# Performance work log

Measured on AMD Instinct MI355X. Metric: run time of the kernel, lower is better.

Reference implementation:

```python
import jax, jax.numpy as jnp
import numpy as np

N = 20000       # nodes
C = 64          # channels per irrep
E = 320000      # edges (avg degree 16)
S = 64          # num_species
R = 8           # radial embedding dim
HR = 64         # radial MLP hidden
HEADS = 2       # readout heads
AVG = 16.0      # avg_num_neighbors
SOFT = 2.0      # soft_normalization


def setup_inputs() -> dict:
    key = jax.random.key(0)
    ks = jax.random.split(key, 28)
    g = lambda k, sh, sc=1.0: jax.random.normal(k, sh, dtype=jnp.float32) * sc
    inv = lambda n: 1.0 / float(np.sqrt(n))
    return {
        "edge_vectors": g(ks[0], (E, 3)),
        "node_feats_s": g(ks[1], (N, C)),
        "node_feats_v": g(ks[2], (N, C, 3)),
        "radial_embeddings": g(ks[3], (E, R)),
        "node_species": jax.random.randint(ks[4], (N,), 0, S),
        "senders": jax.random.randint(ks[5], (E,), 0, N),
        "receivers": jax.random.randint(ks[6], (E,), 0, N),
        # residual FullyConnectedTensorProduct(feats, one-hot species) weights
        "W_rs": g(ks[7], (S, C, C), inv(C)),
        "W_rv": g(ks[8], (S, C, C), inv(C)),
        # interaction: linear up, radial MLP (5 TP paths), linear down
        "W_up_s": g(ks[9], (C, C), inv(C)),
        "W_up_v": g(ks[10], (C, C), inv(C)),
        "Wr1": g(ks[11], (R, HR), inv(R)),
        "Wr2": g(ks[12], (HR, 5 * C), inv(HR)),
        "W_down_s": g(ks[13], (C, C), inv(C)),
        "W_down_v": g(ks[14], (C, C), inv(C)),
        # equivariant product basis: per-channel species-indexed symmetric-contraction weights
        "w1s": g(ks[15], (S, C)),
        "w1v": g(ks[16], (S, C)),
        "w2ss": g(ks[17], (S, C)),
        "w2vv": g(ks[18], (S, C)),
        "w2sv": g(ks[19], (S, C)),
        "W_prod_s": g(ks[20], (C, C), inv(C)),
        "W_prod_v": g(ks[21], (C, C), inv(C)),
        # linear readout heads (out_irreps -> 1x0e per head)
        "w_read": g(ks[22], (HEADS, C), inv(C)),
    }


def reference(edge_vectors, node_feats_s, node_feats_v, radial_embeddings,
              node_species, senders, receivers,
              W_rs, W_rv, W_up_s, W_up_v, Wr1, Wr2, W_down_s, W_down_v,
              w1s, w1v, w2ss, w2vv, w2sv, W_prod_s, W_prod_v, w_read):
    n_nodes = node_feats_s.shape[0]
    sp = node_species

    # --- residual connection: FCTP(feats, one-hot(species)) == species-indexed channel mix
    res_s = jnp.einsum('nc,ncd->nd', node_feats_s, W_rs[sp])
    res_v = jnp.einsum('ncx,ncd->ndx', node_feats_v, W_rv[sp])

    # --- InteractionBlock ---
    s_u = node_feats_s @ W_up_s
    v_u = jnp.einsum('ncx,cd->ndx', node_feats_v, W_up_v)
    nrm = jnp.linalg.norm(edge_vectors, axis=-1, keepdims=True)
    u = edge_vectors / jnp.maximum(nrm, 1e-9)  # l=1 spherical harmonic direction [E,3]
    # radial MLP -> per-edge per-channel weights for the 5 CG paths of (0e+1o)x(0e+1o)->0e+1o
    w = (jax.nn.silu(radial_embeddings @ Wr1) @ Wr2).reshape(-1, 5, s_u.shape[1])
    se = s_u[senders]            # [E,C] gather (irregular)
    ve = v_u[senders]            # [E,C,3]
    dot = jnp.einsum('ecx,ex->ec', ve, u)          # 1o x 1o -> 0e
    crs = jnp.cross(ve, u[:, None, :])             # 1o x 1o -> 1o
    m_s = w[:, 0] * se + w[:, 3] * dot
    m_v = (w[:, 1][..., None] * ve
           + w[:, 2][..., None] * u[:, None, :]
           + w[:, 4][..., None] * crs)
    a_s = jax.ops.segment_sum(m_s, receivers, num_segments=n_nodes) / AVG
    a_v = jax.ops.segment_sum(m_v, receivers, num_segments=n_nodes) / AVG
    a_s = a_s @ W_down_s
    a_v = jnp.einsum('ncx,cd->ndx', a_v, W_down_v)

    # --- EquivariantProductBasisBlock: symmetric contraction (correlation<=2), per-channel
    # species-indexed weights, followed by a linear to out_irreps ---
    vv = jnp.sum(a_v * a_v, axis=-1)                                   # 1o (x) 1o -> 0e
    p_s = w1s[sp] * a_s + w2ss[sp] * a_s * a_s + w2vv[sp] * vv
    p_v = w1v[sp][..., None] * a_v + w2sv[sp][..., None] * a_s[..., None] * a_v
    p_s = p_s @ W_prod_s
    p_v = jnp.einsum('ncx,cd->ndx', p_v, W_prod_v)

    # --- soft normalization: phi(n) = 1/(1 + n*sus(n)), n = norm/SOFT ---
    def sus(x):
        return jnp.where(x > 0, jnp.exp(-1.0 / jnp.where(x > 0, x, 1.0)), 0.0)

    def phi(n):
        n = n / SOFT
        return 1.0 / (1.0 + n * sus(n))

    f_s = p_s * phi(jnp.abs(p_s))
    f_v = p_v * phi(jnp.linalg.norm(p_v, axis=-1, keepdims=True))

    # --- residual add ---
    f_s = f_s + res_s
    f_v = f_v + res_v

    # --- readout heads (Linear out_irreps -> 1x0e), stacked on axis=1 ---
    node_out = jnp.einsum('nc,hc->nh', f_s, w_read)
    return (node_out, f_s, f_v)
```

## Files before the change

### kernel.cpp

```cpp
#include <hip/hip_runtime.h>

#define N_NODES 20000
#define C 64
#define E_EDGES 320000
#define S_SPEC 64
#define R_DIM 8
#define HR 64
#define HEADS 2
#define TE 64
#define NPAIR (E_EDGES/128)
#define HPAD 68
#define INV_AVG (1.0f/16.0f)

#define FS_OFF 40000
#define FV_OFF 1320000

typedef short bf16x4 __attribute__((ext_vector_type(4)));
typedef float f32x4  __attribute__((ext_vector_type(4)));

__device__ __forceinline__ unsigned short f2bf(float f){
  unsigned u = __float_as_uint(f);
  u += 0x7fffu + ((u >> 16) & 1u);
  return (unsigned short)(u >> 16);
}
__device__ __forceinline__ float bf2f(unsigned short b){
  return __uint_as_float(((unsigned)b) << 16);
}
__device__ __forceinline__ unsigned packbf(float a, float b){
  return (unsigned)f2bf(a) | ((unsigned)f2bf(b) << 16);
}
__device__ __forceinline__ float unplo(unsigned u){ return __uint_as_float(u << 16); }
__device__ __forceinline__ float unphi(unsigned u){ return __uint_as_float(u & 0xffff0000u); }
__device__ __forceinline__ float phi_f(float x){
  float n = x * 0.5f;
  float s = (n > 0.0f) ? expf(-1.0f/n) : 0.0f;
  return 1.0f / (1.0f + n * s);
}

__global__ __launch_bounds__(256) void wr2t_kernel(const float* __restrict__ Wr2,
                                                   unsigned short* __restrict__ wr2t){
  int idx = blockIdx.x*256 + threadIdx.x;
  int n = idx >> 6, k = idx & 63;
  wr2t[idx] = f2bf(Wr2[k*320 + n] * INV_AVG);
}

__global__ __launch_bounds__(256) void wpack_kernel(
    const float* __restrict__ W_rs, const float* __restrict__ W_rv,
    const float* __restrict__ W_ds, const float* __restrict__ W_dv,
    const float* __restrict__ W_ps, const float* __restrict__ W_pv,
    const float* __restrict__ Wus,  const float* __restrict__ Wuv,
    unsigned* __restrict__ wrp, unsigned* __restrict__ wdp,
    unsigned* __restrict__ wpp, unsigned* __restrict__ wup){
  int idx = blockIdx.x*256 + threadIdx.x;
  if (idx < S_SPEC*C*C){
    wrp[idx] = packbf(W_rs[idx], W_rv[idx]);
  } else {
    int r = idx - S_SPEC*C*C;
    int which = r >> 12, e = r & 4095;
    if (which == 0)      wdp[e] = packbf(W_ds[e], W_dv[e]);
    else if (which == 1) wpp[e] = packbf(W_ps[e], W_pv[e]);
    else                 wup[e] = packbf(Wus[e],  Wuv[e]);
  }
}

__global__ __launch_bounds__(256) void node_up_kernel(
    const float* __restrict__ fs, const float* __restrict__ fv,
    const unsigned* __restrict__ wup,
    ushort4* __restrict__ suv){
  const int ni = threadIdx.x >> 6;
  const int d  = threadIdx.x & 63;
  const int n  = blockIdx.x*4 + ni;
  __shared__ float s_l[4][C];
  __shared__ float v_l[4][3][C];
  __shared__ unsigned wup_l[C*C];
  const int t = threadIdx.x;
  #pragma unroll
  for (int j = 0; j < 16; ++j) wup_l[t + 256*j] = wup[t + 256*j];
  s_l[ni][d] = fs[n*C + d];
  #pragma unroll
  for (int x = 0; x < 3; ++x) v_l[ni][x][d] = fv[(n*C + d)*3 + x];
  __syncthreads();
  float as = 0.f, a0 = 0.f, a1 = 0.f, a2 = 0.f;
  #pragma unroll 4
  for (int c = 0; c < C; ++c){
    unsigned u = wup_l[c*C + d];
    float wsv = unplo(u);
    float wvv = unphi(u);
    as += s_l[ni][c] * wsv;
    a0 += v_l[ni][0][c] * wvv;
    a1 += v_l[ni][1][c] * wvv;
    a2 += v_l[ni][2][c] * wvv;
  }
  ushort4 o;
  o.x = f2bf(as); o.y = f2bf(a0); o.z = f2bf(a1); o.w = f2bf(a2);
  suv[(size_t)n*C + d] = o;
}

__global__ __launch_bounds__(256) void hist_kernel(const int* __restrict__ rcv, int* __restrict__ count){
  int e = blockIdx.x*256 + threadIdx.x;
  atomicAdd(&count[rcv[e]], 1);
}

__global__ __launch_bounds__(1024) void scan_kernel(const int* __restrict__ count, int* __restrict__ cursor){
  __shared__ int sums[1024];
  const int t = threadIdx.x;
  const int base = t*20;
  int s = 0;
  #pragma unroll 4
  for (int i = 0; i < 20; ++i){ int idx = base+i; if (idx < N_NODES) s += count[idx]; }
  sums[t] = s;
  __syncthreads();
  for (int off = 1; off < 1024; off <<= 1){
    int v = (t >= off) ? sums[t-off] : 0;
    __syncthreads();
    sums[t] += v;
    __syncthreads();
  }
  int run = (t > 0) ? sums[t-1] : 0;
  for (int i = 0; i < 20; ++i){
    int idx = base+i;
    if (idx < N_NODES){ cursor[idx] = run; run += count[idx]; }
  }
}

__global__ __launch_bounds__(256) void scatter_kernel(
    const int* __restrict__ snd, const int* __restrict__ rcv,
    const float* __restrict__ ev, const float* __restrict__ re,
    int* __restrict__ cursor,
    int* __restrict__ snd_s, int* __restrict__ rcv_s,
    float4* __restrict__ u_s, float* __restrict__ re_s){
  int e = blockIdx.x*256 + threadIdx.x;
  int r = rcv[e];
  int pos = atomicAdd(&cursor[r], 1);
  snd_s[pos] = snd[e];
  rcv_s[pos] = r;
  float x = ev[e*3+0], y = ev[e*3+1], z = ev[e*3+2];
  float nr = sqrtf(x*x + y*y + z*z);
  float inv = 1.0f / fmaxf(nr, 1e-9f);
  float4 u4; u4.x = x*inv; u4.y = y*inv; u4.z = z*inv; u4.w = 0.f;
  u_s[pos] = u4;
  const float4* rp = (const float4*)&re[(size_t)e*R_DIM];
  float4 ra = rp[0], rb = rp[1];
  float4* op = (float4*)&re_s[(size_t)pos*R_DIM];
  op[0] = ra; op[1] = rb;
}

__global__ __launch_bounds__(512, 4) void edge_kernel(
    const float4* __restrict__ u_s, const float* __restrict__ re_s,
    const int* __restrict__ snd_s, const int* __restrict__ rcv_s,
    const float* __restrict__ Wr1, const unsigned short* __restrict__ wr2t,
    const ushort4* __restrict__ suv,
    float* __restrict__ a_s, float* __restrict__ a_v)
{
  __shared__ __align__(16) float Wr1_l[R_DIM*HR];
  __shared__ __align__(16) unsigned short Wr2T_l[320*HPAD];

  const int t = threadIdx.x;
  const int lane = t & 63;
  const int w = t >> 6;
  const int g  = w >> 1;
  const int h2 = w & 1;
  int b = blockIdx.x;
  int xcd = b & 7, idx = b >> 3;
  const int q = NPAIR >> 3, r = NPAIR & 7;
  int pair = (xcd < r ? xcd*(q+1) : r*(q+1) + (xcd-r)*q) + idx;
  const int e0A = pair * 128;
  const int e0B = e0A + 64;

  Wr1_l[t] = Wr1[t];
  #pragma unroll
  for (int j = 0; j < 10; ++j){
    int i4 = t + 512*j;
    ushort4 v4 = ((const ushort4*)wr2t)[i4];
    int el = i4*4; int n = el >> 6, k = el & 63;
    *(ushort4*)&Wr2T_l[n*HPAD + k] = v4;
  }

  const int arow = g*16 + (lane & 15);
  const int koff = 4*(lane >> 4);
  const int cl = lane & 15;
  const int ebase = g*16 + (lane >> 4)*4;

  float4 raA = ((const float4*)&re_s[(size_t)(e0A + arow)*R_DIM])[0];
  float4 rbA = ((const float4*)&re_s[(size_t)(e0A + arow)*R_DIM])[1];
  float uxA[4], uyA[4], uzA[4]; int snA[4], rcA[4];
  #pragma unroll
  for (int i = 0; i < 4; ++i){
    int e = e0A + ebase + i;
    float4 uu = u_s[e];
    uxA[i]=uu.x; uyA[i]=uu.y; uzA[i]=uu.z;
    snA[i]=snd_s[e]; rcA[i]=rcv_s[e];
  }
  ushort4 gvA[4][2];
  #pragma unroll
  for (int i = 0; i < 4; ++i){
    const ushort4* sp_ = &suv[(size_t)snA[i]*C];
    #pragma unroll
    for (int kk = 0; kk < 2; ++kk) gvA[i][kk] = sp_[(2*h2 + kk)*16 + cl];
  }
  __syncthreads();

  bf16x4 haA[4];
  #pragma unroll
  for (int kt = 0; kt < 4; ++kt){
    short4 tmp;
    #pragma unroll
    for (int j = 0; j < 4; ++j){
      int k = kt*16 + koff + j;
      float acc = raA.x*Wr1_l[0*HR+k] + raA.y*Wr1_l[1*HR+k] + raA.z*Wr1_l[2*HR+k] + raA.w*Wr1_l[3*HR+k]
                + rbA.x*Wr1_l[4*HR+k] + rbA.y*Wr1_l[5*HR+k] + rbA.z*Wr1_l[6*HR+k] + rbA.w*Wr1_l[7*HR+k];
      float sil = acc / (1.0f + expf(-acc));
      ((unsigned short*)&tmp)[j] = f2bf(sil);
    }
    haA[kt] = *(bf16x4*)&tmp;
  }

  float4 raB = ((const float4*)&re_s[(size_t)(e0B + arow)*R_DIM])[0];
  float4 rbB = ((const float4*)&re_s[(size_t)(e0B + arow)*R_DIM])[1];
  float uxB[4], uyB[4], uzB[4]; int snB[4], rcB[4];
  #pragma unroll
  for (int i = 0; i < 4; ++i){
    int e = e0B + ebase + i;
    float4 uu = u_s[e];
    uxB[i]=uu.x; uyB[i]=uu.y; uzB[i]=uu.z;
    snB[i]=snd_s[e]; rcB[i]=rcv_s[e];
  }

  f32x4 accA[10];
  #pragma unroll
  for (int lf = 0; lf < 10; ++lf) accA[lf] = (f32x4){0.f,0.f,0.f,0.f};
  #pragma unroll
  for (int kt = 0; kt < 4; ++kt){
    bf16x4 af = haA[kt];
    #pragma unroll
    for (int lf = 0; lf < 10; ++lf){
      int p = lf >> 1, kk = lf & 1;
      int n = (p*4 + 2*h2 + kk)*16 + cl;
      bf16x4 bf = *(const bf16x4*)&Wr2T_l[n*HPAD + kt*16 + koff];
      accA[lf] = __builtin_amdgcn_mfma_f32_16x16x16bf16_1k(af, bf, accA[lf], 0, 0, 0);
    }
  }

  ushort4 gvB[4][2];
  #pragma unroll
  for (int i = 0; i < 4; ++i){
    const ushort4* sp_ = &suv[(size_t)snB[i]*C];
    #pragma unroll
    for (int kk = 0; kk < 2; ++kk) gvB[i][kk] = sp_[(2*h2 + kk)*16 + cl];
  }

  {
    float ms[2], mv0[2], mv1[2], mv2[2];
    #pragma unroll
    for (int kk = 0; kk < 2; ++kk){ ms[kk]=0.f; mv0[kk]=0.f; mv1[kk]=0.f; mv2[kk]=0.f; }
    int cur = rcA[0];
    #pragma unroll
    for (int i = 0; i < 4; ++i){
      int rc = rcA[i];
      if (rc != cur){
        #pragma unroll
        for (int kk = 0; kk < 2; ++kk){
          int c = (2*h2 + kk)*16 + cl;
          unsafeAtomicAdd(&a_s[cur*C + c],       ms[kk]);
          unsafeAtomicAdd(&a_v[(cur*3+0)*C + c], mv0[kk]);
          unsafeAtomicAdd(&a_v[(cur*3+1)*C + c], mv1[kk]);
          unsafeAtomicAdd(&a_v[(cur*3+2)*C + c], mv2[kk]);
          ms[kk]=0.f; mv0[kk]=0.f; mv1[kk]=0.f; mv2[kk]=0.f;
        }
        cur = rc;
      }
      float u0 = uxA[i], u1 = uyA[i], u2 = uzA[i];
      #pragma unroll
      for (int kk = 0; kk < 2; ++kk){
        float se  = bf2f(gvA[i][kk].x);
        float ve0 = bf2f(gvA[i][kk].y);
        float ve1 = bf2f(gvA[i][kk].z);
        float ve2 = bf2f(gvA[i][kk].w);
        float w0 = accA[0*2+kk][i];
        float w1 = accA[1*2+kk][i];
        float w2 = accA[2*2+kk][i];
        float w3 = accA[3*2+kk][i];
        float w4 = accA[4*2+kk][i];
        float dt  = ve0*u0 + ve1*u1 + ve2*u2;
        float cr0 = ve1*u2 - ve2*u1;
        float cr1 = ve2*u0 - ve0*u2;
        float cr2 = ve0*u1 - ve1*u0;
        ms[kk]  += w0*se + w3*dt;
        mv0[kk] += w1*ve0 + w2*u0 + w4*cr0;
        mv1[kk] += w1*ve1 + w2*u1 + w4*cr1;
        mv2[kk] += w1*ve2 + w2*u2 + w4*cr2;
      }
    }
    #pragma unroll
    for (int kk = 0; kk < 2; ++kk){
      int c = (2*h2 + kk)*16 + cl;
      unsafeAtomicAdd(&a_s[cur*C + c],       ms[kk]);
      unsafeAtomicAdd(&a_v[(cur*3+0)*C + c], mv0[kk]);
      unsafeAtomicAdd(&a_v[(cur*3+1)*C + c], mv1[kk]);
      unsafeAtomicAdd(&a_v[(cur*3+2)*C + c], mv2[kk]);
    }
  }

  bf16x4 haB[4];
  #pragma unroll
  for (int kt = 0; kt < 4; ++kt){
    short4 tmp;
    #pragma unroll
    for (int j = 0; j < 4; ++j){
      int k = kt*16 + koff + j;
      float acc = raB.x*Wr1_l[0*HR+k] + raB.y*Wr1_l[1*HR+k] + raB.z*Wr1_l[2*HR+k] + raB.w*Wr1_l[3*HR+k]
                + rbB.x*Wr1_l[4*HR+k] + rbB.y*Wr1_l[5*HR+k] + rbB.z*Wr1_l[6*HR+k] + rbB.w*Wr1_l[7*HR+k];
      float sil = acc / (1.0f + expf(-acc));
      ((unsigned short*)&tmp)[j] = f2bf(sil);
    }
    haB[kt] = *(bf16x4*)&tmp;
  }
  f32x4 accB[10];
  #pragma unroll
  for (int lf = 0; lf < 10; ++lf) accB[lf] = (f32x4){0.f,0.f,0.f,0.f};
  #pragma unroll
  for (int kt = 0; kt < 4; ++kt){
    bf16x4 af = haB[kt];
    #pragma unroll
    for (int lf = 0; lf < 10; ++lf){
      int p = lf >> 1, kk = lf & 1;
      int n = (p*4 + 2*h2 + kk)*16 + cl;
      bf16x4 bf = *(const bf16x4*)&Wr2T_l[n*HPAD + kt*16 + koff];
      accB[lf] = __builtin_amdgcn_mfma_f32_16x16x16bf16_1k(af, bf, accB[lf], 0, 0, 0);
    }
  }

  {
    float ms[2], mv0[2], mv1[2], mv2[2];
    #pragma unroll
    for (int kk = 0; kk < 2; ++kk){ ms[kk]=0.f; mv0[kk]=0.f; mv1[kk]=0.f; mv2[kk]=0.f; }
    int cur = rcB[0];
    #pragma unroll
    for (int i = 0; i < 4; ++i){
      int rc = rcB[i];
      if (rc != cur){
        #pragma unroll
        for (int kk = 0; kk < 2; ++kk){
          int c = (2*h2 + kk)*16 + cl;
          unsafeAtomicAdd(&a_s[cur*C + c],       ms[kk]);
          unsafeAtomicAdd(&a_v[(cur*3+0)*C + c], mv0[kk]);
          unsafeAtomicAdd(&a_v[(cur*3+1)*C + c], mv1[kk]);
          unsafeAtomicAdd(&a_v[(cur*3+2)*C + c], mv2[kk]);
          ms[kk]=0.f; mv0[kk]=0.f; mv1[kk]=0.f; mv2[kk]=0.f;
        }
        cur = rc;
      }
      float u0 = uxB[i], u1 = uyB[i], u2 = uzB[i];
      #pragma unroll
      for (int kk = 0; kk < 2; ++kk){
        float se  = bf2f(gvB[i][kk].x);
        float ve0 = bf2f(gvB[i][kk].y);
        float ve1 = bf2f(gvB[i][kk].z);
        float ve2 = bf2f(gvB[i][kk].w);
        float w0 = accB[0*2+kk][i];
        float w1 = accB[1*2+kk][i];
        float w2 = accB[2*2+kk][i];
        float w3 = accB[3*2+kk][i];
        float w4 = accB[4*2+kk][i];
        float dt  = ve0*u0 + ve1*u1 + ve2*u2;
        float cr0 = ve1*u2 - ve2*u1;
        float cr1 = ve2*u0 - ve0*u2;
        float cr2 = ve0*u1 - ve1*u0;
        ms[kk]  += w0*se + w3*dt;
        mv0[kk] += w1*ve0 + w2*u0 + w4*cr0;
        mv1[kk] += w1*ve1 + w2*u1 + w4*cr1;
        mv2[kk] += w1*ve2 + w2*u2 + w4*cr2;
      }
    }
    #pragma unroll
    for (int kk = 0; kk < 2; ++kk){
      int c = (2*h2 + kk)*16 + cl;
      unsafeAtomicAdd(&a_s[cur*C + c],       ms[kk]);
      unsafeAtomicAdd(&a_v[(cur*3+0)*C + c], mv0[kk]);
      unsafeAtomicAdd(&a_v[(cur*3+1)*C + c], mv1[kk]);
      unsafeAtomicAdd(&a_v[(cur*3+2)*C + c], mv2[kk]);
    }
  }
}

__global__ __launch_bounds__(256) void node_post_kernel(
    const float* __restrict__ a_s, const float* __restrict__ a_v,
    const float* __restrict__ fs_in, const float* __restrict__ fv_in,
    const int* __restrict__ species,
    const unsigned* __restrict__ wrp,
    const unsigned* __restrict__ wdp,
    const unsigned* __restrict__ wpp,
    const float* __restrict__ w1s, const float* __restrict__ w1v,
    const float* __restrict__ w2ss, const float* __restrict__ w2vv, const float* __restrict__ w2sv,
    const float* __restrict__ w_read, float* __restrict__ out)
{
  const int ni = threadIdx.x >> 6;
  const int d  = threadIdx.x & 63;
  const int n  = blockIdx.x*4 + ni;
  const int sp = species[n];
  const int t  = threadIdx.x;
  __shared__ float as_l[4][C];
  __shared__ float av_l[4][3][C];
  __shared__ float si_l[4][C];
  __shared__ float vi_l[4][3][C];
  __shared__ unsigned wdp_l[C*C];
  __shared__ unsigned wpp_l[C*C];
  #pragma unroll
  for (int j = 0; j < 16; ++j){
    wdp_l[t + 256*j] = wdp[t + 256*j];
    wpp_l[t + 256*j] = wpp[t + 256*j];
  }
  as_l[ni][d] = a_s[n*C + d];
  #pragma unroll
  for (int x=0;x<3;x++) av_l[ni][x][d] = a_v[(n*3+x)*C + d];
  si_l[ni][d] = fs_in[n*C + d];
  #pragma unroll
  for (int x=0;x<3;x++) vi_l[ni][x][d] = fv_in[(n*C + d)*3 + x];
  __syncthreads();
  const unsigned* wrp_p = wrp + (size_t)sp*C*C;
  float bs=0, bv0=0, bv1=0, bv2=0, rs=0, rv0=0, rv1=0, rv2=0;
  #pragma unroll 4
  for (int c=0;c<C;++c){
    unsigned ud = wdp_l[c*C+d];
    unsigned ur = wrp_p[c*C+d];
    float wds = unplo(ud), wdv = unphi(ud);
    float wrs = unplo(ur), wrv = unphi(ur);
    bs  += as_l[ni][c]*wds;
    bv0 += av_l[ni][0][c]*wdv; bv1 += av_l[ni][1][c]*wdv; bv2 += av_l[ni][2][c]*wdv;
    rs  += si_l[ni][c]*wrs;
    rv0 += vi_l[ni][0][c]*wrv; rv1 += vi_l[ni][1][c]*wrv; rv2 += vi_l[ni][2][c]*wrv;
  }
  float vv = bv0*bv0 + bv1*bv1 + bv2*bv2;
  float ps  = w1s[sp*C+d]*bs + w2ss[sp*C+d]*bs*bs + w2vv[sp*C+d]*vv;
  float c1v = w1v[sp*C+d], c2sv = w2sv[sp*C+d];
  float pv0 = c1v*bv0 + c2sv*bs*bv0;
  float pv1 = c1v*bv1 + c2sv*bs*bv1;
  float pv2 = c1v*bv2 + c2sv*bs*bv2;
  __syncthreads();
  as_l[ni][d] = ps; av_l[ni][0][d]=pv0; av_l[ni][1][d]=pv1; av_l[ni][2][d]=pv2;
  __syncthreads();
  float qs=0, qv0=0, qv1=0, qv2=0;
  #pragma unroll 4
  for (int c=0;c<C;++c){
    unsigned up = wpp_l[c*C+d];
    float wps = unplo(up), wpv = unphi(up);
    qs  += as_l[ni][c]*wps;
    qv0 += av_l[ni][0][c]*wpv; qv1 += av_l[ni][1][c]*wpv; qv2 += av_l[ni][2][c]*wpv;
  }
  float fsv = qs * phi_f(fabsf(qs)) + rs;
  float nv = sqrtf(qv0*qv0 + qv1*qv1 + qv2*qv2);
  float ph = phi_f(nv);
  float fv0 = qv0*ph + rv0;
  float fv1 = qv1*ph + rv1;
  float fv2 = qv2*ph + rv2;
  out[FS_OFF + n*C + d] = fsv;
  float* fvo = &out[FV_OFF + (size_t)(n*C + d)*3];
  fvo[0]=fv0; fvo[1]=fv1; fvo[2]=fv2;
  #pragma unroll
  for (int h=0; h<HEADS; ++h){
    float r = fsv * w_read[h*C + d];
    #pragma unroll
    for (int off=32; off>0; off>>=1) r += __shfl_down(r, off);
    if (d == 0) out[n*HEADS + h] = r;
  }
}

extern "C" void kernel_launch(void* const* d_in, const int* in_sizes, int n_in,
                              void* d_out, int out_size, void* d_ws, size_t ws_size,
                              hipStream_t stream)
{
  const float* ev   = (const float*)d_in[0];
  const float* nfs  = (const float*)d_in[1];
  const float* nfv  = (const float*)d_in[2];
  const float* re   = (const float*)d_in[3];
  const int*   spec = (const int*)d_in[4];
  const int*   snd  = (const int*)d_in[5];
  const int*   rcv  = (const int*)d_in[6];
  const float* W_rs = (const float*)d_in[7];
  const float* W_rv = (const float*)d_in[8];
  const float* Wus  = (const float*)d_in[9];
  const float* Wuv  = (const float*)d_in[10];
  const float* Wr1  = (const float*)d_in[11];
  const float* Wr2  = (const float*)d_in[12];
  const float* Wds  = (const float*)d_in[13];
  const float* Wdv  = (const float*)d_in[14];
  const float* w1s  = (const float*)d_in[15];
  const float* w1v  = (const float*)d_in[16];
  const float* w2ss = (const float*)d_in[17];
  const float* w2vv = (const float*)d_in[18];
  const float* w2sv = (const float*)d_in[19];
  const float* Wps  = (const float*)d_in[20];
  const float* Wpv  = (const float*)d_in[21];
  const float* wrd  = (const float*)d_in[22];

  float* out = (float*)d_out;
  float* ws  = (float*)d_ws;
  ushort4* suv  = (ushort4*)ws;
  float*   a_s  = ws + 2560000;
  float*   a_v  = ws + 3840000;
  int*    count = (int*)(ws + 7680000);
  int*    cursr = (int*)(ws + 7700000);
  int*    snd_s = (int*)(ws + 7720000);
  int*    rcv_s = (int*)(ws + 8040000);
  float4* u_s   = (float4*)(ws + 8360000);
  float*  re_s  = ws + 9640000;
  unsigned short* wr2t = (unsigned short*)(ws + 12200000);
  unsigned* wrp = (unsigned*)(ws + 12210240);
  unsigned* wdp = (unsigned*)(ws + 12472384);
  unsigned* wpp = (unsigned*)(ws + 12476480);
  unsigned* wup = (unsigned*)(ws + 12480576);

  hipMemsetAsync(a_s, 0, (size_t)5120000*sizeof(float), stream);
  hipMemsetAsync(count, 0, (size_t)N_NODES*sizeof(int), stream);

  wr2t_kernel<<<(320*64)/256, 256, 0, stream>>>(Wr2, wr2t);
  wpack_kernel<<<(S_SPEC*C*C + 3*C*C)/256, 256, 0, stream>>>(
      W_rs, W_rv, Wds, Wdv, Wps, Wpv, Wus, Wuv, wrp, wdp, wpp, wup);
  node_up_kernel<<<N_NODES/4, 256, 0, stream>>>(nfs, nfv, wup, suv);
  hist_kernel<<<E_EDGES/256, 256, 0, stream>>>(rcv, count);
  scan_kernel<<<1, 1024, 0, stream>>>(count, cursr);
  scatter_kernel<<<E_EDGES/256, 256, 0, stream>>>(snd, rcv, ev, re, cursr,
                                                  snd_s, rcv_s, u_s, re_s);
  edge_kernel<<<NPAIR, 512, 0, stream>>>(u_s, re_s, snd_s, rcv_s, Wr1, wr2t,
                                         suv, a_s, a_v);
  node_post_kernel<<<N_NODES/4, 256, 0, stream>>>(a_s, a_v, nfs, nfv, spec,
      wrp, wdp, wpp, w1s, w1v, w2ss, w2vv, w2sv, wrd, out);
}
```

Baseline: 392.9 us.

## Fuse prep kernels into one launch, interleave aggregation buffer, shuffle-based scan

Merges the Wr2 transpose, weight packing, receiver histogram and node up-projection into one block-partitioned prep kernel, which removes several launches and lets independent work overlap. The up-projection now reads fp32 weights directly, dropping the packed wup buffer. The per-node scalar and vector aggregates are interleaved as four floats per channel, so the four atomics per channel hit one cache line and node_post reads them as a single float4. The single-block scan replaces its shared-memory Hillis-Steele loop with wavefront shuffles and keeps counts in registers, at the cost of more registers per thread.

```diff
diff --git a/kernel.cpp b/kernel.cpp
--- a/kernel.cpp
+++ b/kernel.cpp
@@ -12,6 +12,12 @@
 #define HPAD 68
 #define INV_AVG (1.0f/16.0f)
 
+#define NB_WR2T 80
+#define NB_WPACK 1056
+#define NB_HIST 1250
+#define NB_NODEUP 5000
+#define PREP_BLOCKS (NB_WR2T + NB_WPACK + NB_HIST + NB_NODEUP)
+
 #define FS_OFF 40000
 #define FV_OFF 1320000
 
@@ -37,89 +43,112 @@
   return 1.0f / (1.0f + n * s);
 }
 
-__global__ __launch_bounds__(256) void wr2t_kernel(const float* __restrict__ Wr2,
-                                                   unsigned short* __restrict__ wr2t){
-  int idx = blockIdx.x*256 + threadIdx.x;
-  int n = idx >> 6, k = idx & 63;
-  wr2t[idx] = f2bf(Wr2[k*320 + n] * INV_AVG);
-}
-
-__global__ __launch_bounds__(256) void wpack_kernel(
+__global__ __launch_bounds__(256) void prep_kernel(
+    const float* __restrict__ Wr2, unsigned short* __restrict__ wr2t,
     const float* __restrict__ W_rs, const float* __restrict__ W_rv,
     const float* __restrict__ W_ds, const float* __restrict__ W_dv,
     const float* __restrict__ W_ps, const float* __restrict__ W_pv,
-    const float* __restrict__ Wus,  const float* __restrict__ Wuv,
-    unsigned* __restrict__ wrp, unsigned* __restrict__ wdp,
-    unsigned* __restrict__ wpp, unsigned* __restrict__ wup){
-  int idx = blockIdx.x*256 + threadIdx.x;
-  if (idx < S_SPEC*C*C){
-    wrp[idx] = packbf(W_rs[idx], W_rv[idx]);
-  } else {
-    int r = idx - S_SPEC*C*C;
-    int which = r >> 12, e = r & 4095;
-    if (which == 0)      wdp[e] = packbf(W_ds[e], W_dv[e]);
-    else if (which == 1) wpp[e] = packbf(W_ps[e], W_pv[e]);
-    else                 wup[e] = packbf(Wus[e],  Wuv[e]);
-  }
-}
-
-__global__ __launch_bounds__(256) void node_up_kernel(
+    unsigned* __restrict__ wrp, unsigned* __restrict__ wdp, unsigned* __restrict__ wpp,
+    const int* __restrict__ rcv, int* __restrict__ count,
     const float* __restrict__ fs, const float* __restrict__ fv,
-    const unsigned* __restrict__ wup,
-    ushort4* __restrict__ suv){
-  const int ni = threadIdx.x >> 6;
-  const int d  = threadIdx.x & 63;
-  const int n  = blockIdx.x*4 + ni;
-  __shared__ float s_l[4][C];
-  __shared__ float v_l[4][3][C];
-  __shared__ unsigned wup_l[C*C];
+    const float* __restrict__ Wus, const float* __restrict__ Wuv,
+    ushort4* __restrict__ suv)
+{
+  const int b = blockIdx.x;
   const int t = threadIdx.x;
-  #pragma unroll
-  for (int j = 0; j < 16; ++j) wup_l[t + 256*j] = wup[t + 256*j];
-  s_l[ni][d] = fs[n*C + d];
-  #pragma unroll
-  for (int x = 0; x < 3; ++x) v_l[ni][x][d] = fv[(n*C + d)*3 + x];
-  __syncthreads();
-  float as = 0.f, a0 = 0.f, a1 = 0.f, a2 = 0.f;
-  #pragma unroll 4
-  for (int c = 0; c < C; ++c){
-    unsigned u = wup_l[c*C + d];
-    float wsv = unplo(u);
-    float wvv = unphi(u);
-    as += s_l[ni][c] * wsv;
-    a0 += v_l[ni][0][c] * wvv;
-    a1 += v_l[ni][1][c] * wvv;
-    a2 += v_l[ni][2][c] * wvv;
-  }
-  ushort4 o;
-  o.x = f2bf(as); o.y = f2bf(a0); o.z = f2bf(a1); o.w = f2bf(a2);
-  suv[(size_t)n*C + d] = o;
-}
-
-__global__ __launch_bounds__(256) void hist_kernel(const int* __restrict__ rcv, int* __restrict__ count){
-  int e = blockIdx.x*256 + threadIdx.x;
-  atomicAdd(&count[rcv[e]], 1);
+  if (b < NB_WR2T){
+    int idx = b*256 + t;
+    int n = idx >> 6, k = idx & 63;
+    wr2t[idx] = f2bf(Wr2[k*320 + n] * INV_AVG);
+    return;
+  }
+  if (b < NB_WR2T + NB_WPACK){
+    int idx = (b - NB_WR2T)*256 + t;
+    if (idx < S_SPEC*C*C){
+      wrp[idx] = packbf(W_rs[idx], W_rv[idx]);
+    } else {
+      int r2 = idx - S_SPEC*C*C;
+      if (r2 < 4096) wdp[r2] = packbf(W_ds[r2], W_dv[r2]);
+      else           wpp[r2-4096] = packbf(W_ps[r2-4096], W_pv[r2-4096]);
+    }
+    return;
+  }
+  if (b < NB_WR2T + NB_WPACK + NB_HIST){
+    int e = (b - NB_WR2T - NB_WPACK)*256 + t;
+    atomicAdd(&count[rcv[e]], 1);
+    return;
+  }
+  {
+    __shared__ float wus_l[C*C];
+    __shared__ float wuv_l[C*C];
+    __shared__ float s_l[4][C];
+    __shared__ float v_l[4][3][C];
+    const int nb = b - (NB_WR2T + NB_WPACK + NB_HIST);
+    const int ni = t >> 6;
+    const int d  = t & 63;
+    const int n  = nb*4 + ni;
+    #pragma unroll
+    for (int j = 0; j < 16; ++j){
+      wus_l[t + 256*j] = Wus[t + 256*j];
+      wuv_l[t + 256*j] = Wuv[t + 256*j];
+    }
+    s_l[ni][d] = fs[n*C + d];
+    #pragma unroll
+    for (int x = 0; x < 3; ++x) v_l[ni][x][d] = fv[(n*C + d)*3 + x];
+    __syncthreads();
+    float as = 0.f, a0 = 0.f, a1 = 0.f, a2 = 0.f;
+    #pragma unroll 4
+    for (int c = 0; c < C; ++c){
+      float wsv = wus_l[c*C + d];
+      float wvv = wuv_l[c*C + d];
+      as += s_l[ni][c] * wsv;
+      a0 += v_l[ni][0][c] * wvv;
+      a1 += v_l[ni][1][c] * wvv;
+      a2 += v_l[ni][2][c] * wvv;
+    }
+    ushort4 o;
+    o.x = f2bf(as); o.y = f2bf(a0); o.z = f2bf(a1); o.w = f2bf(a2);
+    suv[(size_t)n*C + d] = o;
+  }
 }
 
 __global__ __launch_bounds__(1024) void scan_kernel(const int* __restrict__ count, int* __restrict__ cursor){
-  __shared__ int sums[1024];
+  __shared__ int wsum[16];
   const int t = threadIdx.x;
+  const int lane = t & 63, wid = t >> 6;
   const int base = t*20;
   int s = 0;
+  int loc[20];
   #pragma unroll 4
-  for (int i = 0; i < 20; ++i){ int idx = base+i; if (idx < N_NODES) s += count[idx]; }
-  sums[t] = s;
-  __syncthreads();
-  for (int off = 1; off < 1024; off <<= 1){
-    int v = (t >= off) ? sums[t-off] : 0;
-    __syncthreads();
-    sums[t] += v;
-    __syncthreads();
-  }
-  int run = (t > 0) ? sums[t-1] : 0;
   for (int i = 0; i < 20; ++i){
     int idx = base+i;
-    if (idx < N_NODES){ cursor[idx] = run; run += count[idx]; }
+    int v = (idx < N_NODES) ? count[idx] : 0;
+    loc[i] = v; s += v;
+  }
+  int x = s;
+  #pragma unroll
+  for (int dlt = 1; dlt < 64; dlt <<= 1){
+    int y = __shfl_up(x, dlt);
+    if (lane >= dlt) x += y;
+  }
+  if (lane == 63) wsum[wid] = x;
+  __syncthreads();
+  if (wid == 0 && lane < 16){
+    int w = wsum[lane];
+    #pragma unroll
+    for (int dlt = 1; dlt < 16; dlt <<= 1){
+      int y = __shfl_up(w, dlt);
+      if (lane >= dlt) w += y;
+    }
+    wsum[lane] = w;
+  }
+  __syncthreads();
+  int wpre = (wid > 0) ? wsum[wid-1] : 0;
+  int run = wpre + (x - s);
+  #pragma unroll 4
+  for (int i = 0; i < 20; ++i){
+    int idx = base+i;
+    if (idx < N_NODES){ cursor[idx] = run; run += loc[i]; }
   }
 }
 
@@ -150,7 +179,7 @@
     const int* __restrict__ snd_s, const int* __restrict__ rcv_s,
     const float* __restrict__ Wr1, const unsigned short* __restrict__ wr2t,
     const ushort4* __restrict__ suv,
-    float* __restrict__ a_s, float* __restrict__ a_v)
+    float* __restrict__ a_sv)
 {
   __shared__ __align__(16) float Wr1_l[R_DIM*HR];
   __shared__ __align__(16) unsigned short Wr2T_l[320*HPAD];
@@ -261,10 +290,11 @@
         #pragma unroll
         for (int kk = 0; kk < 2; ++kk){
           int c = (2*h2 + kk)*16 + cl;
-          unsafeAtomicAdd(&a_s[cur*C + c],       ms[kk]);
-          unsafeAtomicAdd(&a_v[(cur*3+0)*C + c], mv0[kk]);
-          unsafeAtomicAdd(&a_v[(cur*3+1)*C + c], mv1[kk]);
-          unsafeAtomicAdd(&a_v[(cur*3+2)*C + c], mv2[kk]);
+          float* dst = &a_sv[((size_t)cur*C + c)*4];
+          unsafeAtomicAdd(dst+0, ms[kk]);
+          unsafeAtomicAdd(dst+1, mv0[kk]);
+          unsafeAtomicAdd(dst+2, mv1[kk]);
+          unsafeAtomicAdd(dst+3, mv2[kk]);
           ms[kk]=0.f; mv0[kk]=0.f; mv1[kk]=0.f; mv2[kk]=0.f;
         }
         cur = rc;
@@ -294,10 +324,11 @@
     #pragma unroll
     for (int kk = 0; kk < 2; ++kk){
       int c = (2*h2 + kk)*16 + cl;
-      unsafeAtomicAdd(&a_s[cur*C + c],       ms[kk]);
-      unsafeAtomicAdd(&a_v[(cur*3+0)*C + c], mv0[kk]);
-      unsafeAtomicAdd(&a_v[(cur*3+1)*C + c], mv1[kk]);
-      unsafeAtomicAdd(&a_v[(cur*3+2)*C + c], mv2[kk]);
+      float* dst = &a_sv[((size_t)cur*C + c)*4];
+      unsafeAtomicAdd(dst+0, ms[kk]);
+      unsafeAtomicAdd(dst+1, mv0[kk]);
+      unsafeAtomicAdd(dst+2, mv1[kk]);
+      unsafeAtomicAdd(dst+3, mv2[kk]);
     }
   }
 
@@ -342,10 +373,11 @@
         #pragma unroll
         for (int kk = 0; kk < 2; ++kk){
           int c = (2*h2 + kk)*16 + cl;
-          unsafeAtomicAdd(&a_s[cur*C + c],       ms[kk]);
-          unsafeAtomicAdd(&a_v[(cur*3+0)*C + c], mv0[kk]);
-          unsafeAtomicAdd(&a_v[(cur*3+1)*C + c], mv1[kk]);
-          unsafeAtomicAdd(&a_v[(cur*3+2)*C + c], mv2[kk]);
+          float* dst = &a_sv[((size_t)cur*C + c)*4];
+          unsafeAtomicAdd(dst+0, ms[kk]);
+          unsafeAtomicAdd(dst+1, mv0[kk]);
+          unsafeAtomicAdd(dst+2, mv1[kk]);
+          unsafeAtomicAdd(dst+3, mv2[kk]);
           ms[kk]=0.f; mv0[kk]=0.f; mv1[kk]=0.f; mv2[kk]=0.f;
         }
         cur = rc;
@@ -375,16 +407,17 @@
     #pragma unroll
     for (int kk = 0; kk < 2; ++kk){
       int c = (2*h2 + kk)*16 + cl;
-      unsafeAtomicAdd(&a_s[cur*C + c],       ms[kk]);
-      unsafeAtomicAdd(&a_v[(cur*3+0)*C + c], mv0[kk]);
-      unsafeAtomicAdd(&a_v[(cur*3+1)*C + c], mv1[kk]);
-      unsafeAtomicAdd(&a_v[(cur*3+2)*C + c], mv2[kk]);
+      float* dst = &a_sv[((size_t)cur*C + c)*4];
+      unsafeAtomicAdd(dst+0, ms[kk]);
+      unsafeAtomicAdd(dst+1, mv0[kk]);
+      unsafeAtomicAdd(dst+2, mv1[kk]);
+      unsafeAtomicAdd(dst+3, mv2[kk]);
     }
   }
 }
 
 __global__ __launch_bounds__(256) void node_post_kernel(
-    const float* __restrict__ a_s, const float* __restrict__ a_v,
+    const float* __restrict__ a_sv,
     const float* __restrict__ fs_in, const float* __restrict__ fv_in,
     const int* __restrict__ species,
     const unsigned* __restrict__ wrp,
@@ -410,9 +443,11 @@
     wdp_l[t + 256*j] = wdp[t + 256*j];
     wpp_l[t + 256*j] = wpp[t + 256*j];
   }
-  as_l[ni][d] = a_s[n*C + d];
-  #pragma unroll
-  for (int x=0;x<3;x++) av_l[ni][x][d] = a_v[(n*3+x)*C + d];
+  {
+    float4 av = ((const float4*)a_sv)[(size_t)n*C + d];
+    as_l[ni][d] = av.x;
+    av_l[ni][0][d] = av.y; av_l[ni][1][d] = av.z; av_l[ni][2][d] = av.w;
+  }
   si_l[ni][d] = fs_in[n*C + d];
   #pragma unroll
   for (int x=0;x<3;x++) vi_l[ni][x][d] = fv_in[(n*C + d)*3 + x];
@@ -496,8 +531,7 @@
   float* out = (float*)d_out;
   float* ws  = (float*)d_ws;
   ushort4* suv  = (ushort4*)ws;
-  float*   a_s  = ws + 2560000;
-  float*   a_v  = ws + 3840000;
+  float*   a_sv = ws + 2560000;
   int*    count = (int*)(ws + 7680000);
   int*    cursr = (int*)(ws + 7700000);
   int*    snd_s = (int*)(ws + 7720000);
@@ -508,21 +542,18 @@
   unsigned* wrp = (unsigned*)(ws + 12210240);
   unsigned* wdp = (unsigned*)(ws + 12472384);
   unsigned* wpp = (unsigned*)(ws + 12476480);
-  unsigned* wup = (unsigned*)(ws + 12480576);
-
-  hipMemsetAsync(a_s, 0, (size_t)5120000*sizeof(float), stream);
+
+  hipMemsetAsync(a_sv, 0, (size_t)5120000*sizeof(float), stream);
   hipMemsetAsync(count, 0, (size_t)N_NODES*sizeof(int), stream);
 
-  wr2t_kernel<<<(320*64)/256, 256, 0, stream>>>(Wr2, wr2t);
-  wpack_kernel<<<(S_SPEC*C*C + 3*C*C)/256, 256, 0, stream>>>(
-      W_rs, W_rv, Wds, Wdv, Wps, Wpv, Wus, Wuv, wrp, wdp, wpp, wup);
-  node_up_kernel<<<N_NODES/4, 256, 0, stream>>>(nfs, nfv, wup, suv);
-  hist_kernel<<<E_EDGES/256, 256, 0, stream>>>(rcv, count);
+  prep_kernel<<<PREP_BLOCKS, 256, 0, stream>>>(
+      Wr2, wr2t, W_rs, W_rv, Wds, Wdv, Wps, Wpv, wrp, wdp, wpp,
+      rcv, count, nfs, nfv, Wus, Wuv, suv);
   scan_kernel<<<1, 1024, 0, stream>>>(count, cursr);
   scatter_kernel<<<E_EDGES/256, 256, 0, stream>>>(snd, rcv, ev, re, cursr,
                                                   snd_s, rcv_s, u_s, re_s);
   edge_kernel<<<NPAIR, 512, 0, stream>>>(u_s, re_s, snd_s, rcv_s, Wr1, wr2t,
-                                         suv, a_s, a_v);
-  node_post_kernel<<<N_NODES/4, 256, 0, stream>>>(a_s, a_v, nfs, nfv, spec,
+                                         suv, a_sv);
+  node_post_kernel<<<N_NODES/4, 256, 0, stream>>>(a_sv, nfs, nfv, spec,
       wrp, wdp, wpp, w1s, w1v, w2ss, w2vv, w2sv, wrd, out);
 }
```

Result: slower. 558.3 us (+42.1%).
